# Performance work log

Measured on AMD Instinct MI355X. Metric: run time of the kernel, lower is better.

Reference implementation:

```python
import jax, jax.numpy as jnp
import numpy as np

N = 50000
NEG_SLOPE = 0.2


def _gat_layer(x, W, a_src, a_dst, b, src, dst, heads, out_dim):
    # Linear transform per head: [N, heads, out]
    h = (x @ W).reshape(N, heads, out_dim)
    # Per-node attention halves (PyG: att applied to [x_i || x_j])
    alpha_s = jnp.einsum('nho,ho->nh', h, a_src)  # source/message half
    alpha_d = jnp.einsum('nho,ho->nh', h, a_dst)  # destination half
    # Per-edge logits with leaky relu, [E, heads]
    e = jax.nn.leaky_relu(alpha_s[src] + alpha_d[dst], negative_slope=NEG_SLOPE)
    # Segment softmax over edges sharing the same destination node
    m = jax.ops.segment_max(e, dst, num_segments=N)
    m = jax.lax.stop_gradient(m)
    ex = jnp.exp(e - m[dst])
    denom = jax.ops.segment_sum(ex, dst, num_segments=N)
    coef = ex / denom[dst]                         # [E, heads]
    # Weighted scatter-aggregate of source messages
    msg = h[src] * coef[:, :, None]                # [E, heads, out]
    agg = jax.ops.segment_sum(msg, dst, num_segments=N)
    return agg.reshape(N, heads * out_dim) + b


def _add_self_loops(edge_index):
    loops = jnp.arange(N, dtype=edge_index.dtype)
    src = jnp.concatenate([edge_index[0], loops])
    dst = jnp.concatenate([edge_index[1], loops])
    return src, dst


def setup_inputs() -> dict:
    key = jax.random.key(0)
    ks = jax.random.split(key, 9)
    E = 800000
    x = jax.random.normal(ks[0], (N, 128), dtype=jnp.float32)
    edge_index = jax.random.randint(ks[1], (2, E), 0, N, dtype=jnp.int64)
    # Glorot-ish scaled params
    W1 = jax.random.normal(ks[2], (128, 64), dtype=jnp.float32) * (1.0 / np.sqrt(128))
    a1_src = jax.random.normal(ks[3], (8, 8), dtype=jnp.float32) * 0.3
    a1_dst = jax.random.normal(ks[4], (8, 8), dtype=jnp.float32) * 0.3
    b1 = jnp.zeros((64,), dtype=jnp.float32)
    W2 = jax.random.normal(ks[5], (64, 40), dtype=jnp.float32) * (1.0 / np.sqrt(64))
    a2_src = jax.random.normal(ks[6], (1, 40), dtype=jnp.float32) * 0.3
    a2_dst = jax.random.normal(ks[7], (1, 40), dtype=jnp.float32) * 0.3
    b2 = jnp.zeros((40,), dtype=jnp.float32)
    return {"x": x, "edge_index": edge_index, "W1": W1, "a1_src": a1_src,
            "a1_dst": a1_dst, "b1": b1, "W2": W2, "a2_src": a2_src,
            "a2_dst": a2_dst, "b2": b2}


def reference(x, edge_index, W1, a1_src, a1_dst, b1, W2, a2_src, a2_dst, b2):
    # Eval mode: all F.dropout(p=0.6) calls are identity.
    src, dst = _add_self_loops(edge_index)
    h = _gat_layer(x, W1, a1_src, a1_dst, b1, src, dst, heads=8, out_dim=8)
    h = jax.nn.elu(h)
    h = _gat_layer(h, W2, a2_src, a2_dst, b2, src, dst, heads=1, out_dim=40)
    return jax.nn.log_softmax(h, axis=1)
```

## Files before the change

kernel.cpp:

```cpp
#include <hip/hip_runtime.h>
#include <hip/hip_bf16.h>
#include <math.h>

#define N_NODES 50000
#define E_EDGES 800000
#define E_TOT   850000
#define NEG_SLOPE 0.2f
#define SCAN_BLOCKS 49
#define BUCKETS 512
#define RNG 98
#define FA_CHUNK 16384
#define FA_THREADS 512
#define FA_EPT (FA_CHUNK / FA_THREADS)

__global__ __launch_bounds__(256) void k_detect0(const unsigned int* __restrict__ ei,
                                                 int* __restrict__ flag,
                                                 int* __restrict__ offs) {
    int gid = blockIdx.x * 256 + threadIdx.x;
    for (int i = gid; i <= N_NODES; i += gridDim.x * 256) offs[i] = 0;
    if (blockIdx.x == 0) {
        __shared__ int anynz;
        if (threadIdx.x == 0) anynz = 0;
        __syncthreads();
        int nz = 0;
        for (int i = threadIdx.x; i < 2048; i += 256)
            nz |= (ei[2 * i + 1] != 0u);
        if (nz) atomicOr(&anynz, 1);
        __syncthreads();
        if (threadIdx.x == 0) *flag = (anynz == 0) ? 1 : 0;
    }
}

__device__ __forceinline__ void edge_nodes(const void* ei, int is64, int e, int& s, int& d) {
    if (e >= E_EDGES) { s = d = e - E_EDGES; return; }
    if (is64) {
        const long long* p = (const long long*)ei;
        s = (int)p[e]; d = (int)p[E_EDGES + e];
    } else {
        const int* p = (const int*)ei;
        s = p[e]; d = p[E_EDGES + e];
    }
}

__global__ void k_count(const void* __restrict__ ei, const int* __restrict__ flag,
                        int* __restrict__ counts) {
    int e = blockIdx.x * 256 + threadIdx.x;
    if (e >= E_TOT) return;
    int s, d;
    edge_nodes(ei, *flag, e, s, d);
    atomicAdd(&counts[d], 1);
}

__global__ __launch_bounds__(1024) void k_scanA(int* __restrict__ offs,
                                                int* __restrict__ partials) {
    __shared__ int lds[1024];
    const int t   = threadIdx.x;
    const int idx = blockIdx.x * 1024 + t;
    int v = (idx <= N_NODES) ? offs[idx] : 0;
    lds[t] = v;
    __syncthreads();
    for (int off = 1; off < 1024; off <<= 1) {
        int u = (t >= off) ? lds[t - off] : 0;
        __syncthreads();
        lds[t] += u;
        __syncthreads();
    }
    int incl = lds[t];
    if (idx <= N_NODES) offs[idx] = incl - v;
    if (t == 1023) partials[blockIdx.x] = incl;
}

__global__ __launch_bounds__(1024) void k_scanC(int* __restrict__ offs,
                                                const int* __restrict__ partials,
                                                int* __restrict__ cursor,
                                                int* __restrict__ bcur) {
    __shared__ int sprefix;
    const int t   = threadIdx.x;
    const int bid = blockIdx.x;
    if (t < 64) {
        int p = (t < bid) ? partials[t] : 0;
#pragma unroll
        for (int off = 32; off; off >>= 1) p += __shfl_down(p, off);
        if (t == 0) sprefix = p;
    }
    __syncthreads();
    const int idx = bid * 1024 + t;
    if (idx <= N_NODES) {
        int v = offs[idx] + sprefix;
        offs[idx] = v;
        if (idx < N_NODES) cursor[idx] = v;
        if ((idx % RNG) == 0 && idx < N_NODES) bcur[idx / RNG] = v;
        if (idx == N_NODES) bcur[BUCKETS - 1] = v;
    }
}

__global__ __launch_bounds__(FA_THREADS) void k_fillA(const void* __restrict__ ei,
                                                      const int* __restrict__ flag,
                                                      int* __restrict__ bcur,
                                                      unsigned int* __restrict__ stage) {
    __shared__ int cnt[BUCKETS];
    __shared__ int base[BUCKETS];
    __shared__ int lofs[BUCKETS];
    const int t  = threadIdx.x;
    const int cb = blockIdx.x * FA_CHUNK;
    const int is64 = *flag;
    cnt[t] = 0;
    __syncthreads();
    unsigned int pk[FA_EPT];
#pragma unroll
    for (int i = 0; i < FA_EPT; ++i) {
        int e = cb + i * FA_THREADS + t;
        pk[i] = 0xFFFFFFFFu;
        if (e < E_TOT) {
            int s, d;
            edge_nodes(ei, is64, e, s, d);
            pk[i] = ((unsigned)d << 16) | (unsigned)s;
            atomicAdd(&cnt[(unsigned)d / RNG], 1);
        }
    }
    __syncthreads();
    {
        int c = cnt[t];
        base[t] = c ? atomicAdd(&bcur[t], c) : 0;
        lofs[t] = 0;
    }
    __syncthreads();
#pragma unroll
    for (int i = 0; i < FA_EPT; ++i) {
        if (pk[i] != 0xFFFFFFFFu) {
            int b  = (pk[i] >> 16) / RNG;
            int lp = atomicAdd(&lofs[b], 1);
            stage[base[b] + lp] = pk[i];
        }
    }
}

__global__ __launch_bounds__(256) void k_fillB(const unsigned int* __restrict__ stage,
                                               const int* __restrict__ offs,
                                               int* __restrict__ cursor,
                                               int* __restrict__ csr) {
    const int b = blockIdx.x;
    const int t = threadIdx.x;
    if (b == 0 && t < 16) csr[E_TOT + t] = 0;
    const int lo  = b * RNG;
    const int hi  = min(lo + RNG, N_NODES);
    const int rb0 = offs[lo];
    const int rb1 = offs[hi];
    for (int i = rb0 + t; i < rb1; i += 256) {
        unsigned int v = stage[i];
        int d   = (int)(v >> 16);
        int pos = atomicAdd(&cursor[d], 1);
        csr[pos] = (int)(v & 0xFFFFu);
    }
}

__global__ __launch_bounds__(256) void k1_transform(
        const float* __restrict__ x, const float* __restrict__ W1,
        const float* __restrict__ a1s, const float* __restrict__ a1d,
        float* __restrict__ h1, float* __restrict__ as1, float* __restrict__ ad1) {
    __shared__ float ws[128 * 64];
    __shared__ float xs[64 * 132];
    const int t  = threadIdx.x;
    const int nb = blockIdx.x * 64;
    for (int i = t * 4; i < 128 * 64; i += 1024)
        *(float4*)&ws[i] = *(const float4*)&W1[i];
    for (int i = t * 4; i < 64 * 128; i += 1024) {
        int n = i >> 7, k = i & 127;
        float4 v = make_float4(0.f, 0.f, 0.f, 0.f);
        if (nb + n < N_NODES) v = *(const float4*)&x[(size_t)(nb + n) * 128 + k];
        *(float4*)&xs[n * 132 + k] = v;
    }
    __syncthreads();

    const int oq = t & 15;
    const int nq = t >> 4;
    float4 acc[4];
#pragma unroll
    for (int i = 0; i < 4; ++i) acc[i] = make_float4(0.f, 0.f, 0.f, 0.f);

    for (int k = 0; k < 128; k += 4) {
        float4 wv0 = *(float4*)&ws[(k + 0) * 64 + oq * 4];
        float4 wv1 = *(float4*)&ws[(k + 1) * 64 + oq * 4];
        float4 wv2 = *(float4*)&ws[(k + 2) * 64 + oq * 4];
        float4 wv3 = *(float4*)&ws[(k + 3) * 64 + oq * 4];
#pragma unroll
        for (int i = 0; i < 4; ++i) {
            float4 xv = *(float4*)&xs[(nq * 4 + i) * 132 + k];
            acc[i].x += xv.x * wv0.x + xv.y * wv1.x + xv.z * wv2.x + xv.w * wv3.x;
            acc[i].y += xv.x * wv0.y + xv.y * wv1.y + xv.z * wv2.y + xv.w * wv3.y;
            acc[i].z += xv.x * wv0.z + xv.y * wv1.z + xv.z * wv2.z + xv.w * wv3.z;
            acc[i].w += xv.x * wv0.w + xv.y * wv1.w + xv.z * wv2.w + xv.w * wv3.w;
        }
    }
    __syncthreads();
#pragma unroll
    for (int i = 0; i < 4; ++i) {
        int n = nq * 4 + i;
        *(float4*)&xs[n * 68 + oq * 4] = acc[i];
        if (nb + n < N_NODES)
            *(float4*)&h1[(size_t)(nb + n) * 64 + oq * 4] = acc[i];
    }
    __syncthreads();
    for (int p = t; p < 512; p += 256) {
        int n = p >> 3, hd = p & 7;
        float ss = 0.f, dd = 0.f;
#pragma unroll
        for (int o = 0; o < 8; ++o) {
            float hv = xs[n * 68 + hd * 8 + o];
            ss += hv * a1s[hd * 8 + o];
            dd += hv * a1d[hd * 8 + o];
        }
        if (nb + n < N_NODES) {
            as1[(nb + n) * 8 + hd] = ss;
            ad1[(nb + n) * 8 + hd] = dd;
        }
    }
}

__global__ __launch_bounds__(256) void k_agg1f(
        const float* __restrict__ h1, const float* __restrict__ as1g,
        const float* __restrict__ ad1g, const int* __restrict__ offs,
        const int* __restrict__ csr, const float* __restrict__ b1,
        const float* __restrict__ W2, const float* __restrict__ a2s,
        const float* __restrict__ a2d,
        float* __restrict__ h2p, float* __restrict__ as2, float* __restrict__ ad2) {
    __shared__ float ws[64 * 40];
    __shared__ float rows[4][64];
    const int t = threadIdx.x;
    for (int i = t; i < 64 * 40; i += 256) ws[i] = W2[i];
    __syncthreads();

    const int w = t >> 6, l = t & 63;
    const int wid = blockIdx.x * 4 + w;
    if (wid >= N_NODES) return;
    const int hd = l >> 3;
    const float ad = ad1g[wid * 8 + hd];
    const int j0 = __builtin_amdgcn_readfirstlane(offs[wid]);
    const int j1 = __builtin_amdgcn_readfirstlane(offs[wid + 1]);

    float a[8], g[8];
    int   cn[8];
    {
        int c0[8];
#pragma unroll
        for (int i = 0; i < 8; ++i) c0[i] = csr[j0 + i];
#pragma unroll
        for (int i = 0; i < 8; ++i) a[i] = as1g[(unsigned)c0[i] * 8u + (unsigned)hd];
#pragma unroll
        for (int i = 0; i < 8; ++i) g[i] = h1[(unsigned)c0[i] * 64u + (unsigned)l];
#pragma unroll
        for (int i = 0; i < 8; ++i) cn[i] = csr[j0 + 8 + i];
    }

    float den0 = 0.f, den1 = 0.f, acc0 = 0.f, acc1 = 0.f;
    int j = j0;
    while (j + 8 <= j1) {
        float au[8], gu[8];
#pragma unroll
        for (int i = 0; i < 8; ++i) { au[i] = a[i]; gu[i] = g[i]; }
#pragma unroll
        for (int i = 0; i < 8; ++i) a[i] = as1g[(unsigned)cn[i] * 8u + (unsigned)hd];
#pragma unroll
        for (int i = 0; i < 8; ++i) g[i] = h1[(unsigned)cn[i] * 64u + (unsigned)l];
#pragma unroll
        for (int i = 0; i < 8; ++i) cn[i] = csr[j + 16 + i];
#pragma unroll
        for (int i = 0; i < 8; ++i) {
            float e = au[i] + ad;
            e = fmaxf(e, NEG_SLOPE * e);
            float xp = __expf(e);
            if (i & 1) { den1 += xp; acc1 = fmaf(xp, gu[i], acc1); }
            else       { den0 += xp; acc0 = fmaf(xp, gu[i], acc0); }
        }
        j += 8;
    }
    const int rem = j1 - j;
    if (rem) {
#pragma unroll
        for (int i = 0; i < 8; ++i) {
            float e = a[i] + ad;
            e = fmaxf(e, NEG_SLOPE * e);
            float xp = (i < rem) ? __expf(e) : 0.f;
            if (i & 1) { den1 += xp; acc1 = fmaf(xp, g[i], acc1); }
            else       { den0 += xp; acc0 = fmaf(xp, g[i], acc0); }
        }
    }

    float v = (acc0 + acc1) / (den0 + den1) + b1[l];
    v = (v > 0.f) ? v : expm1f(v);
    rows[w][l] = v;

    float acc2 = 0.f;
    if (l < 40) {
#pragma unroll 8
        for (int k = 0; k < 64; ++k)
            acc2 = fmaf(rows[w][k], ws[k * 40 + l], acc2);
    }
    float ps = (l < 40) ? acc2 * a2s[l] : 0.f;
    float pd = (l < 40) ? acc2 * a2d[l] : 0.f;
#pragma unroll
    for (int off = 32; off; off >>= 1) {
        ps += __shfl_down(ps, off);
        pd += __shfl_down(pd, off);
    }
    if (l < 40) h2p[(unsigned)wid * 48u + (unsigned)l] = acc2;
    if (l == 0) { as2[wid] = ps; ad2[wid] = pd; }
}

__global__ __launch_bounds__(256) void k_agg2(
        const float* __restrict__ h2p, const float* __restrict__ as2,
        const float* __restrict__ ad2, const int* __restrict__ offs,
        const int* __restrict__ csr, const float* __restrict__ b2,
        float* __restrict__ out) {
    int wid = (blockIdx.x * 256 + threadIdx.x) >> 6;
    int l   = threadIdx.x & 63;
    if (wid >= N_NODES) return;
    const bool act = (l < 40);
    const float ad = ad2[wid];
    const int j0 = __builtin_amdgcn_readfirstlane(offs[wid]);
    const int j1 = __builtin_amdgcn_readfirstlane(offs[wid + 1]);

    float a[8], g[8];
    int   cn[8];
    {
        int c0[8];
#pragma unroll
        for (int i = 0; i < 8; ++i) c0[i] = csr[j0 + i];
#pragma unroll
        for (int i = 0; i < 8; ++i) a[i] = as2[c0[i]];
#pragma unroll
        for (int i = 0; i < 8; ++i) g[i] = act ? h2p[(unsigned)c0[i] * 48u + (unsigned)l] : 0.f;
#pragma unroll
        for (int i = 0; i < 8; ++i) cn[i] = csr[j0 + 8 + i];
    }

    float den0 = 0.f, den1 = 0.f, acc0 = 0.f, acc1 = 0.f;
    int j = j0;
    while (j + 8 <= j1) {
        float au[8], gu[8];
#pragma unroll
        for (int i = 0; i < 8; ++i) { au[i] = a[i]; gu[i] = g[i]; }
#pragma unroll
        for (int i = 0; i < 8; ++i) a[i] = as2[cn[i]];
#pragma unroll
        for (int i = 0; i < 8; ++i) g[i] = act ? h2p[(unsigned)cn[i] * 48u + (unsigned)l] : 0.f;
#pragma unroll
        for (int i = 0; i < 8; ++i) cn[i] = csr[j + 16 + i];
#pragma unroll
        for (int i = 0; i < 8; ++i) {
            float e = au[i] + ad;
            e = fmaxf(e, NEG_SLOPE * e);
            float xp = __expf(e);
            if (i & 1) { den1 += xp; acc1 = fmaf(xp, gu[i], acc1); }
            else       { den0 += xp; acc0 = fmaf(xp, gu[i], acc0); }
        }
        j += 8;
    }
    const int rem = j1 - j;
    if (rem) {
#pragma unroll
        for (int i = 0; i < 8; ++i) {
            float e = a[i] + ad;
            e = fmaxf(e, NEG_SLOPE * e);
            float xp = (i < rem) ? __expf(e) : 0.f;
            if (i & 1) { den1 += xp; acc1 = fmaf(xp, g[i], acc1); }
            else       { den0 += xp; acc0 = fmaf(xp, g[i], acc0); }
        }
    }

    float v = act ? ((acc0 + acc1) / (den0 + den1) + b2[l]) : -1e30f;
    float m = v;
#pragma unroll
    for (int off = 32; off; off >>= 1) m = fmaxf(m, __shfl_xor(m, off));
    float ex2 = act ? __expf(v - m) : 0.f;
    float s2 = ex2;
#pragma unroll
    for (int off = 32; off; off >>= 1) s2 += __shfl_xor(s2, off);
    if (act) out[(size_t)wid * 40 + l] = v - m - __logf(s2);
}

extern "C" void kernel_launch(void* const* d_in, const int* in_sizes, int n_in,
                              void* d_out, int out_size, void* d_ws, size_t ws_size,
                              hipStream_t stream) {
    const float* x   = (const float*)d_in[0];
    const void*  ei  = d_in[1];
    const float* W1  = (const float*)d_in[2];
    const float* a1s = (const float*)d_in[3];
    const float* a1d = (const float*)d_in[4];
    const float* b1  = (const float*)d_in[5];
    const float* W2  = (const float*)d_in[6];
    const float* a2s = (const float*)d_in[7];
    const float* a2d = (const float*)d_in[8];
    const float* b2  = (const float*)d_in[9];
    float* out = (float*)d_out;

    float* fws = (float*)d_ws;
    float* h1  = fws + 0;
    float* as1 = fws + 3200000;
    float* ad1 = fws + 3600000;
    float* h2p = fws + 4000000;
    float* as2 = fws + 6400000;
    float* ad2 = fws + 6450000;
    int*   offs     = (int*)(fws + 6500000);
    int*   cursor   = offs + (N_NODES + 1);
    int*   csr      = cursor + N_NODES;
    int*   partials = csr + E_TOT + 16;
    int*   flag     = partials + SCAN_BLOCKS;
    int*   bcur     = flag + 1;
    unsigned int* stage = (unsigned int*)(bcur + BUCKETS);

    k_detect0<<<64, 256, 0, stream>>>((const unsigned int*)ei, flag, offs);

    int egrid = (E_TOT + 255) / 256;
    k_count<<<egrid, 256, 0, stream>>>(ei, flag, offs);
    k_scanA<<<SCAN_BLOCKS, 1024, 0, stream>>>(offs, partials);
    k_scanC<<<SCAN_BLOCKS, 1024, 0, stream>>>(offs, partials, cursor, bcur);

    int fagrid = (E_TOT + FA_CHUNK - 1) / FA_CHUNK;
    k_fillA<<<fagrid, FA_THREADS, 0, stream>>>(ei, flag, bcur, stage);
    k_fillB<<<BUCKETS - 1, 256, 0, stream>>>(stage, offs, cursor, csr);

    k1_transform<<<(N_NODES + 63) / 64, 256, 0, stream>>>(x, W1, a1s, a1d, h1, as1, ad1);

    int ngrid = (N_NODES + 3) / 4;
    k_agg1f<<<ngrid, 256, 0, stream>>>(h1, as1, ad1, offs, csr, b1,
                                       W2, a2s, a2d, h2p, as2, ad2);
    k_agg2<<<ngrid, 256, 0, stream>>>(h2p, as2, ad2, offs, csr, b2, out);
}
```

Baseline: 295.8 us.

## Vectorize GAT aggregation with float4 gathers and 4 edges per wavefront

Both aggregation kernels now split each 64-lane wavefront into four 16-lane groups. Each group handles a different edge and loads the neighbor feature row as float4, and the partial sums are reduced across groups with shuffles at the end. This replaces the 8-deep per-lane prefetch of scalar loads with wider vector gathers, meant to cut load instruction count and raise useful bytes per request. The edge count kernel also stops loading the unused source index. In exchange the software prefetch depth per lane is lower, and there is extra cross-lane reduction work.

After: 302.9 us. 2.4% more time.

```diff
diff --git a/kernel.cpp b/kernel.cpp
--- a/kernel.cpp
+++ b/kernel.cpp
@@ -46,8 +46,10 @@
                         int* __restrict__ counts) {
     int e = blockIdx.x * 256 + threadIdx.x;
     if (e >= E_TOT) return;
-    int s, d;
-    edge_nodes(ei, *flag, e, s, d);
+    int d;
+    if (e >= E_EDGES) d = e - E_EDGES;
+    else if (*flag)   d = (int)((const long long*)ei)[E_EDGES + e];
+    else              d = ((const int*)ei)[E_EDGES + e];
     atomicAdd(&counts[d], 1);
 }
 
@@ -231,64 +233,69 @@
     __syncthreads();
 
     const int w = t >> 6, l = t & 63;
+    const int q = l >> 4;
+    const int r = l & 15;
+    const int h = r >> 1;
     const int wid = blockIdx.x * 4 + w;
     if (wid >= N_NODES) return;
-    const int hd = l >> 3;
-    const float ad = ad1g[wid * 8 + hd];
+    const float ad = ad1g[wid * 8 + h];
     const int j0 = __builtin_amdgcn_readfirstlane(offs[wid]);
     const int j1 = __builtin_amdgcn_readfirstlane(offs[wid + 1]);
 
-    float a[8], g[8];
-    int   cn[8];
-    {
-        int c0[8];
-#pragma unroll
-        for (int i = 0; i < 8; ++i) c0[i] = csr[j0 + i];
-#pragma unroll
-        for (int i = 0; i < 8; ++i) a[i] = as1g[(unsigned)c0[i] * 8u + (unsigned)hd];
-#pragma unroll
-        for (int i = 0; i < 8; ++i) g[i] = h1[(unsigned)c0[i] * 64u + (unsigned)l];
-#pragma unroll
-        for (int i = 0; i < 8; ++i) cn[i] = csr[j0 + 8 + i];
-    }
-
-    float den0 = 0.f, den1 = 0.f, acc0 = 0.f, acc1 = 0.f;
+    float den = 0.f;
+    float4 acc = make_float4(0.f, 0.f, 0.f, 0.f);
+
+    int c = csr[j0 + q];
+    float  a = as1g[(unsigned)c * 8u + (unsigned)h];
+    float4 g = *(const float4*)&h1[(unsigned)c * 64u + (unsigned)r * 4u];
+    int cn = csr[j0 + 4 + q];
     int j = j0;
-    while (j + 8 <= j1) {
-        float au[8], gu[8];
-#pragma unroll
-        for (int i = 0; i < 8; ++i) { au[i] = a[i]; gu[i] = g[i]; }
-#pragma unroll
-        for (int i = 0; i < 8; ++i) a[i] = as1g[(unsigned)cn[i] * 8u + (unsigned)hd];
-#pragma unroll
-        for (int i = 0; i < 8; ++i) g[i] = h1[(unsigned)cn[i] * 64u + (unsigned)l];
-#pragma unroll
-        for (int i = 0; i < 8; ++i) cn[i] = csr[j + 16 + i];
-#pragma unroll
-        for (int i = 0; i < 8; ++i) {
-            float e = au[i] + ad;
-            e = fmaxf(e, NEG_SLOPE * e);
-            float xp = __expf(e);
-            if (i & 1) { den1 += xp; acc1 = fmaf(xp, gu[i], acc1); }
-            else       { den0 += xp; acc0 = fmaf(xp, gu[i], acc0); }
-        }
-        j += 8;
+    while (j + 4 <= j1) {
+        float  an = as1g[(unsigned)cn * 8u + (unsigned)h];
+        float4 gn = *(const float4*)&h1[(unsigned)cn * 64u + (unsigned)r * 4u];
+        int cnn = csr[j + 8 + q];
+        float e = a + ad;
+        e = fmaxf(e, NEG_SLOPE * e);
+        float xp = __expf(e);
+        den += xp;
+        acc.x = fmaf(xp, g.x, acc.x);
+        acc.y = fmaf(xp, g.y, acc.y);
+        acc.z = fmaf(xp, g.z, acc.z);
+        acc.w = fmaf(xp, g.w, acc.w);
+        a = an; g = gn; cn = cnn;
+        j += 4;
     }
     const int rem = j1 - j;
     if (rem) {
-#pragma unroll
-        for (int i = 0; i < 8; ++i) {
-            float e = a[i] + ad;
-            e = fmaxf(e, NEG_SLOPE * e);
-            float xp = (i < rem) ? __expf(e) : 0.f;
-            if (i & 1) { den1 += xp; acc1 = fmaf(xp, g[i], acc1); }
-            else       { den0 += xp; acc0 = fmaf(xp, g[i], acc0); }
-        }
-    }
-
-    float v = (acc0 + acc1) / (den0 + den1) + b1[l];
-    v = (v > 0.f) ? v : expm1f(v);
-    rows[w][l] = v;
+        float e = a + ad;
+        e = fmaxf(e, NEG_SLOPE * e);
+        float xp = (q < rem) ? __expf(e) : 0.f;
+        den += xp;
+        acc.x = fmaf(xp, g.x, acc.x);
+        acc.y = fmaf(xp, g.y, acc.y);
+        acc.z = fmaf(xp, g.z, acc.z);
+        acc.w = fmaf(xp, g.w, acc.w);
+    }
+#pragma unroll
+    for (int m = 16; m <= 32; m <<= 1) {
+        den   += __shfl_xor(den,   m);
+        acc.x += __shfl_xor(acc.x, m);
+        acc.y += __shfl_xor(acc.y, m);
+        acc.z += __shfl_xor(acc.z, m);
+        acc.w += __shfl_xor(acc.w, m);
+    }
+    const float inv = 1.0f / den;
+    float4 bv = *(const float4*)&b1[r * 4];
+    float4 v;
+    v.x = fmaf(acc.x, inv, bv.x);
+    v.y = fmaf(acc.y, inv, bv.y);
+    v.z = fmaf(acc.z, inv, bv.z);
+    v.w = fmaf(acc.w, inv, bv.w);
+    v.x = (v.x > 0.f) ? v.x : expm1f(v.x);
+    v.y = (v.y > 0.f) ? v.y : expm1f(v.y);
+    v.z = (v.z > 0.f) ? v.z : expm1f(v.z);
+    v.w = (v.w > 0.f) ? v.w : expm1f(v.w);
+    if (q == 0) *(float4*)&rows[w][r * 4] = v;
 
     float acc2 = 0.f;
     if (l < 40) {
@@ -315,68 +322,79 @@
     int wid = (blockIdx.x * 256 + threadIdx.x) >> 6;
     int l   = threadIdx.x & 63;
     if (wid >= N_NODES) return;
-    const bool act = (l < 40);
+    const int q = l >> 4;
+    const int r = l & 15;
+    const bool act = (r < 10);
     const float ad = ad2[wid];
     const int j0 = __builtin_amdgcn_readfirstlane(offs[wid]);
     const int j1 = __builtin_amdgcn_readfirstlane(offs[wid + 1]);
 
-    float a[8], g[8];
-    int   cn[8];
-    {
-        int c0[8];
-#pragma unroll
-        for (int i = 0; i < 8; ++i) c0[i] = csr[j0 + i];
-#pragma unroll
-        for (int i = 0; i < 8; ++i) a[i] = as2[c0[i]];
-#pragma unroll
-        for (int i = 0; i < 8; ++i) g[i] = act ? h2p[(unsigned)c0[i] * 48u + (unsigned)l] : 0.f;
-#pragma unroll
-        for (int i = 0; i < 8; ++i) cn[i] = csr[j0 + 8 + i];
-    }
-
-    float den0 = 0.f, den1 = 0.f, acc0 = 0.f, acc1 = 0.f;
+    float den = 0.f;
+    float4 acc = make_float4(0.f, 0.f, 0.f, 0.f);
+
+    int c = csr[j0 + q];
+    float  a = as2[c];
+    float4 g = act ? *(const float4*)&h2p[(unsigned)c * 48u + (unsigned)r * 4u]
+                   : make_float4(0.f, 0.f, 0.f, 0.f);
+    int cn = csr[j0 + 4 + q];
     int j = j0;
-    while (j + 8 <= j1) {
-        float au[8], gu[8];
-#pragma unroll
-        for (int i = 0; i < 8; ++i) { au[i] = a[i]; gu[i] = g[i]; }
-#pragma unroll
-        for (int i = 0; i < 8; ++i) a[i] = as2[cn[i]];
-#pragma unroll
-        for (int i = 0; i < 8; ++i) g[i] = act ? h2p[(unsigned)cn[i] * 48u + (unsigned)l] : 0.f;
-#pragma unroll
-        for (int i = 0; i < 8; ++i) cn[i] = csr[j + 16 + i];
-#pragma unroll
-        for (int i = 0; i < 8; ++i) {
-            float e = au[i] + ad;
-            e = fmaxf(e, NEG_SLOPE * e);
-            float xp = __expf(e);
-            if (i & 1) { den1 += xp; acc1 = fmaf(xp, gu[i], acc1); }
-            else       { den0 += xp; acc0 = fmaf(xp, gu[i], acc0); }
-        }
-        j += 8;
+    while (j + 4 <= j1) {
+        float  an = as2[cn];
+        float4 gn = act ? *(const float4*)&h2p[(unsigned)cn * 48u + (unsigned)r * 4u]
+                        : make_float4(0.f, 0.f, 0.f, 0.f);
+        int cnn = csr[j + 8 + q];
+        float e = a + ad;
+        e = fmaxf(e, NEG_SLOPE * e);
+        float xp = __expf(e);
+        den += xp;
+        acc.x = fmaf(xp, g.x, acc.x);
+        acc.y = fmaf(xp, g.y, acc.y);
+        acc.z = fmaf(xp, g.z, acc.z);
+        acc.w = fmaf(xp, g.w, acc.w);
+        a = an; g = gn; cn = cnn;
+        j += 4;
     }
     const int rem = j1 - j;
     if (rem) {
-#pragma unroll
-        for (int i = 0; i < 8; ++i) {
-            float e = a[i] + ad;
-            e = fmaxf(e, NEG_SLOPE * e);
-            float xp = (i < rem) ? __expf(e) : 0.f;
-            if (i & 1) { den1 += xp; acc1 = fmaf(xp, g[i], acc1); }
-            else       { den0 += xp; acc0 = fmaf(xp, g[i], acc0); }
-        }
-    }
-
-    float v = act ? ((acc0 + acc1) / (den0 + den1) + b2[l]) : -1e30f;
-    float m = v;
-#pragma unroll
-    for (int off = 32; off; off >>= 1) m = fmaxf(m, __shfl_xor(m, off));
-    float ex2 = act ? __expf(v - m) : 0.f;
-    float s2 = ex2;
-#pragma unroll
-    for (int off = 32; off; off >>= 1) s2 += __shfl_xor(s2, off);
-    if (act) out[(size_t)wid * 40 + l] = v - m - __logf(s2);
+        float e = a + ad;
+        e = fmaxf(e, NEG_SLOPE * e);
+        float xp = (q < rem) ? __expf(e) : 0.f;
+        den += xp;
+        acc.x = fmaf(xp, g.x, acc.x);
+        acc.y = fmaf(xp, g.y, acc.y);
+        acc.z = fmaf(xp, g.z, acc.z);
+        acc.w = fmaf(xp, g.w, acc.w);
+    }
+#pragma unroll
+    for (int m = 16; m <= 32; m <<= 1) {
+        den   += __shfl_xor(den,   m);
+        acc.x += __shfl_xor(acc.x, m);
+        acc.y += __shfl_xor(acc.y, m);
+        acc.z += __shfl_xor(acc.z, m);
+        acc.w += __shfl_xor(acc.w, m);
+    }
+    const float inv = 1.0f / den;
+    float4 v = make_float4(0.f, 0.f, 0.f, 0.f);
+    if (act) {
+        float4 bv = *(const float4*)&b2[r * 4];
+        v.x = fmaf(acc.x, inv, bv.x);
+        v.y = fmaf(acc.y, inv, bv.y);
+        v.z = fmaf(acc.z, inv, bv.z);
+        v.w = fmaf(acc.w, inv, bv.w);
+    }
+    float mx = act ? fmaxf(fmaxf(v.x, v.y), fmaxf(v.z, v.w)) : -1e30f;
+#pragma unroll
+    for (int m = 1; m <= 8; m <<= 1) mx = fmaxf(mx, __shfl_xor(mx, m));
+    float s = act ? (__expf(v.x - mx) + __expf(v.y - mx) +
+                     __expf(v.z - mx) + __expf(v.w - mx)) : 0.f;
+#pragma unroll
+    for (int m = 1; m <= 8; m <<= 1) s += __shfl_xor(s, m);
+    const float lg = mx + __logf(s);
+    if (act && q == 0) {
+        float4 o;
+        o.x = v.x - lg; o.y = v.y - lg; o.z = v.z - lg; o.w = v.w - lg;
+        *(float4*)&out[(size_t)wid * 40 + r * 4] = o;
+    }
 }
 
 extern "C" void kernel_launch(void* const* d_in, const int* in_sizes, int n_in,
```
